# Kernel optimization log

Hardware: AMD Instinct MI355X
Metric: run time of the kernel (lower is better)

Reference implementation:

```python
import jax, jax.numpy as jnp
import numpy as np

BETA = 0.9       # membrane decay factor
THRESHOLD = 1.0  # firing threshold
ALPHA = 2.0      # atan surrogate slope (snntorch default)

@jax.custom_vjp
def spike(x):
    # Heaviside spike on (mem - threshold)
    return (x > 0).astype(x.dtype)

def _spike_fwd(x):
    return (x > 0).astype(x.dtype), x

def _spike_bwd(x, g):
    # atan surrogate: d spk / d x = (alpha/2) / (1 + (pi/2 * alpha * x)^2)
    return (g * (ALPHA / 2.0) / (1.0 + (jnp.pi / 2.0 * ALPHA * x) ** 2),)

spike.defvjp(_spike_fwd, _spike_bwd)


def snn_forward(x, params):
    """x: (T, B, F_in); params: list of (W[out,in], b[out]).
    Returns (spike_record (T,B,out), final membrane (B,out)).
    Dropout is identity (eval mode). LIF: mem=beta*mem+cur; spk=H(mem-thr); mem-=spk*thr."""
    B = x.shape[1]
    mems0 = tuple(jnp.zeros((B, W.shape[0]), x.dtype) for W, _ in params)

    def step(mems, xt):
        h = xt
        new_mems = []
        for (W, b), m in zip(params, mems):
            cur = h @ W.T + b                 # (B, out)
            m = BETA * m + cur                # leaky integrate
            s = spike(m - THRESHOLD)          # fire
            m = m - s * THRESHOLD             # subtract reset
            new_mems.append(m)
            h = s                             # spikes feed next layer
        return tuple(new_mems), (h, new_mems[-1])

    _, (spks, mem_rec) = jax.lax.scan(step, mems0, x)
    return spks, mem_rec[-1]


def _linear_init(key, out_f, in_f):
    k1, k2 = jax.random.split(key)
    bound = 1.0 / np.sqrt(in_f)
    W = jax.random.uniform(k1, (out_f, in_f), jnp.float32, -bound, bound)
    b = jax.random.uniform(k2, (out_f,), jnp.float32, -bound, bound)
    return W, b


def setup_inputs() -> dict:
    key = jax.random.key(0)
    ks = jax.random.split(key, 4)
    T, B = 25, 256
    sizes = [1024, 2048, 2048, 1024]
    x = jax.random.normal(ks[0], (T, B, sizes[0]), jnp.float32)
    w0, b0 = _linear_init(ks[1], sizes[1], sizes[0])
    w1, b1 = _linear_init(ks[2], sizes[2], sizes[1])
    w2, b2 = _linear_init(ks[3], sizes[3], sizes[2])
    return {"x": x, "w0": w0, "b0": b0, "w1": w1, "b1": b1, "w2": w2, "b2": b2}


def reference(x, w0, b0, w1, b1, w2, b2):
    return snn_forward(x, [(w0, b0), (w1, b1), (w2, b2)])
```

## Files before the change

### kernel.cpp

```cpp
#include <hip/hip_runtime.h>
#include <hip/hip_bf16.h>

typedef __bf16 bf16;
typedef __bf16 bf16x4 __attribute__((ext_vector_type(4)));
typedef __bf16 bf16x8 __attribute__((ext_vector_type(8)));
typedef float  f32x4  __attribute__((ext_vector_type(4)));

#define DEVFN static __device__ __forceinline__

static constexpr int T_STEPS = 25;
static constexpr int BATCH   = 256;
static constexpr int MROWS   = T_STEPS * BATCH;

DEVFN void llds16(const void* g, void* l) {
    __builtin_amdgcn_global_load_lds(
        (const __attribute__((address_space(1))) void*)g,
        (__attribute__((address_space(3))) void*)l, 16, 0, 0);
}

DEVFN void split3_chunk(const float* src, bf16* p0, bf16* p1, bf16* p2, int i) {
    float4 v = *(const float4*)(src + i);
    float vv[4] = {v.x, v.y, v.z, v.w};
    bf16x4 a, b, c;
#pragma unroll
    for (int k = 0; k < 4; ++k) {
        bf16 h0 = (bf16)vv[k];
        float r1 = vv[k] - (float)h0;
        bf16 h1 = (bf16)r1;
        float r2 = r1 - (float)h1;
        a[k] = h0; b[k] = h1; c[k] = (bf16)r2;
    }
    *(bf16x4*)(p0 + i) = a;
    *(bf16x4*)(p1 + i) = b;
    *(bf16x4*)(p2 + i) = c;
}

DEVFN void split2_chunk(const float* src, bf16* p0, bf16* p1, int i) {
    float4 v = *(const float4*)(src + i);
    float vv[4] = {v.x, v.y, v.z, v.w};
    bf16x4 a, b;
#pragma unroll
    for (int k = 0; k < 4; ++k) {
        bf16 h0 = (bf16)vv[k];
        a[k] = h0; b[k] = (bf16)(vv[k] - (float)h0);
    }
    *(bf16x4*)(p0 + i) = a;
    *(bf16x4*)(p1 + i) = b;
}

static constexpr int SB_W0 = 2048;
static constexpr int SB_W1 = 4096;
static constexpr int SB_W2 = 2048;
static constexpr int SB_X  = 6400;

__global__ void split_all(const float* __restrict__ w0, bf16* w0p0, bf16* w0p1, bf16* w0p2,
                          const float* __restrict__ w1, bf16* w1p0, bf16* w1p1, bf16* w1p2,
                          const float* __restrict__ w2, bf16* w2p0, bf16* w2p1,
                          const float* __restrict__ x,  bf16* xp0,  bf16* xp1,  bf16* xp2) {
    int b = blockIdx.x;
    if (b < SB_W0) {
        split3_chunk(w0, w0p0, w0p1, w0p2, b * 1024 + threadIdx.x * 4);
    } else if (b < SB_W0 + SB_W1) {
        split3_chunk(w1, w1p0, w1p1, w1p2, (b - SB_W0) * 1024 + threadIdx.x * 4);
    } else if (b < SB_W0 + SB_W1 + SB_W2) {
        split2_chunk(w2, w2p0, w2p1, (b - SB_W0 - SB_W1) * 1024 + threadIdx.x * 4);
    } else {
        split3_chunk(x, xp0, xp1, xp2, (b - SB_W0 - SB_W1 - SB_W2) * 1024 + threadIdx.x * 4);
    }
}


struct TileCtx { int t, lane, wm, wn, bm, bn, fr, fkS, fk64a, fk64b, cr, cc; };

DEVFN TileCtx make_ctx512() {
    TileCtx x;
    x.t = threadIdx.x; x.lane = x.t & 63;
    int wv = x.t >> 6;
    x.wm = (wv >> 1) * 64;
    x.wn = (wv & 1) * 64;
    x.bm = blockIdx.x * 256; x.bn = blockIdx.y * 128;
    x.fr  = x.lane & 15;
    int g = x.lane >> 4;
    x.fkS   = (g ^ ((x.lane >> 1) & 3)) * 16;
    x.fk64a = ((0 * 4 + g) ^ (x.lane & 7)) * 16;
    x.fk64b = ((1 * 4 + g) ^ (x.lane & 7)) * 16;
    x.cr = (x.lane >> 4) * 4; x.cc = x.lane & 15;
    return x;
}

template <int ROWS, int BK>
DEVFN void stageP(const bf16* g, bf16* s, int base_row, int K, int k0, int t) {
    constexpr int CPR  = BK / 8;
    constexpr int ITER = ROWS * CPR / 512;
#pragma unroll
    for (int r = 0; r < ITER; ++r) {
        int c    = t + r * 512;
        int row  = c / CPR;
        int slot = c % CPR;
        int src  = (BK == 32) ? (slot ^ ((row >> 1) & 3))
                              : (slot ^ (row & 7));
        llds16(g + (size_t)(base_row + row) * K + k0 + src * 8,
               (bf16*)((char*)s + (c >> 6) * 1024));
    }
}

template <int BK>
DEVFN void frag4(bf16x8* f, const bf16* s, int wrow, int fr, int fkS) {
#pragma unroll
    for (int i = 0; i < 4; ++i)
        f[i] = *(const bf16x8*)((const char*)s + (wrow + i * 16 + fr) * (2 * BK) + fkS);
}

DEVFN void mfma16(f32x4 (&acc)[4][4], const bf16x8* a, const bf16x8* b) {
#pragma unroll
    for (int i = 0; i < 4; ++i)
#pragma unroll
        for (int j = 0; j < 4; ++j)
            acc[i][j] = __builtin_amdgcn_mfma_f32_16x16x32_bf16(a[i], b[j], acc[i][j], 0, 0, 0);
}

DEVFN void epilogue(const f32x4 (&accM)[4][4], const f32x4 (&accS)[4][4],
                    const float* bias, float* C, int N, const TileCtx& x) {
#pragma unroll
    for (int j = 0; j < 4; ++j) {
        int col   = x.bn + x.wn + j * 16 + x.cc;
        double bv = (double)bias[col];
#pragma unroll
        for (int i = 0; i < 4; ++i) {
            int row0 = x.bm + x.wm + i * 16 + x.cr;
#pragma unroll
            for (int r = 0; r < 4; ++r) {
                double v = (double)accM[i][j][r] + (double)accS[i][j][r] + bv;
                C[(size_t)(row0 + r) * N + col] = (float)v;
            }
        }
    }
}

template <int MODE>
__global__ __launch_bounds__(512, 2)
void gemm_ph(const bf16* __restrict__ A0, const bf16* __restrict__ A1,
             const bf16* __restrict__ A2, const bf16* __restrict__ B0,
             const bf16* __restrict__ B1, const bf16* __restrict__ B2,
             const float* __restrict__ bias, float* __restrict__ C,
             int M, int N, int K) {
    constexpr int BK  = (MODE == 0) ? 32 : 64;
    constexpr int NA  = (MODE == 0) ? 3 : 1;
    constexpr int NB  = (MODE == 2) ? 2 : 3;
    constexpr int APL = 256 * BK;
    constexpr int BPL = 128 * BK;
    constexpr int BUF = NA * APL + NB * BPL;
    __shared__ __align__(1024) bf16 lds[2 * BUF];

    TileCtx x = make_ctx512();
    f32x4 accM[4][4] = {}, accS[4][4] = {};

    auto pA = [&](int p, int i) { return lds + p * BUF + i * APL; };
    auto pB = [&](int p, int i) { return lds + p * BUF + NA * APL + i * BPL; };

    auto stage_all = [&](int p, int k0) {
        stageP<256, BK>(A0, pA(p, 0), x.bm, K, k0, x.t);
        if constexpr (MODE == 0) {
            stageP<256, BK>(A1, pA(p, 1), x.bm, K, k0, x.t);
            stageP<256, BK>(A2, pA(p, 2), x.bm, K, k0, x.t);
        }
        stageP<128, BK>(B0, pB(p, 0), x.bn, K, k0, x.t);
        stageP<128, BK>(B1, pB(p, 1), x.bn, K, k0, x.t);
        if constexpr (NB == 3) stageP<128, BK>(B2, pB(p, 2), x.bn, K, k0, x.t);
    };

    stage_all(0, 0);
    __syncthreads();

    const int NT = K / BK;
    int p = 0;
    for (int tt = 0; tt < NT; ++tt, p ^= 1) {
        if (tt + 1 < NT) stage_all(p ^ 1, (tt + 1) * BK);

        bf16x8 a[4], b0f[4], b1f[4], b2f[4];
        if constexpr (MODE == 0) {
            frag4<32>(a,   pA(p, 0), x.wm, x.fr, x.fkS);
            frag4<32>(b0f, pB(p, 0), x.wn, x.fr, x.fkS);
            mfma16(accM, a, b0f);
            frag4<32>(b1f, pB(p, 1), x.wn, x.fr, x.fkS);
            mfma16(accS, a, b1f);
            frag4<32>(b2f, pB(p, 2), x.wn, x.fr, x.fkS);
            mfma16(accS, a, b2f);
            frag4<32>(a, pA(p, 1), x.wm, x.fr, x.fkS);
            mfma16(accS, a, b0f);
            mfma16(accS, a, b1f);
            frag4<32>(a, pA(p, 2), x.wm, x.fr, x.fkS);
            mfma16(accS, a, b0f);
        } else {
#pragma unroll
            for (int kh = 0; kh < 2; ++kh) {
                const int fk = kh ? x.fk64b : x.fk64a;
                frag4<64>(a,   pA(p, 0), x.wm, x.fr, fk);
                frag4<64>(b0f, pB(p, 0), x.wn, x.fr, fk);
                mfma16(accM, a, b0f);
                frag4<64>(b1f, pB(p, 1), x.wn, x.fr, fk);
                mfma16(accS, a, b1f);
                if constexpr (NB == 3) {
                    frag4<64>(b2f, pB(p, 2), x.wn, x.fr, fk);
                    mfma16(accS, a, b2f);
                }
            }
        }
        __syncthreads();
    }
    epilogue(accM, accS, bias, C, N, x);
}

template <int F>
__global__ void lif_hidden(const float* __restrict__ cur, bf16* __restrict__ spk) {
    const int tid = blockIdx.x * 256 + threadIdx.x;
    double m = 0.0;
    size_t off = tid;
#pragma unroll
    for (int t = 0; t < T_STEPS; ++t) {
        m = 0.9 * m + (double)cur[off];
        bool s = (m - 1.0) > 0.0;
        spk[off] = (bf16)(s ? 1.0f : 0.0f);
        if (s) m -= 1.0;
        off += (size_t)BATCH * F;
    }
}

__global__ void lif_out(const float* __restrict__ cur, float* __restrict__ out) {
    const int tid = blockIdx.x * 256 + threadIdx.x;
    double m = 0.0;
    size_t off = tid;
#pragma unroll
    for (int t = 0; t < T_STEPS; ++t) {
        m = 0.9 * m + (double)cur[off];
        bool s = (m - 1.0) > 0.0;
        out[off] = s ? 1.0f : 0.0f;
        if (s) m -= 1.0;
        off += (size_t)BATCH * 1024;
    }
    out[(size_t)T_STEPS * BATCH * 1024 + tid] = (float)m;
}

extern "C" void kernel_launch(void* const* d_in, const int* in_sizes, int n_in,
                              void* d_out, int out_size, void* d_ws, size_t ws_size,
                              hipStream_t stream) {
    const float* xin = (const float*)d_in[0];
    const float* w0  = (const float*)d_in[1];
    const float* b0  = (const float*)d_in[2];
    const float* w1  = (const float*)d_in[3];
    const float* b1  = (const float*)d_in[4];
    const float* w2  = (const float*)d_in[5];
    const float* b2  = (const float*)d_in[6];
    float* out = (float*)d_out;

    constexpr size_t NW0 = 2048 * 1024;
    constexpr size_t NW1 = 2048 * 2048;
    constexpr size_t NW2 = 1024 * 2048;
    constexpr size_t NX  = (size_t)MROWS * 1024;
    constexpr size_t NH  = (size_t)MROWS * 2048;

    char* ws = (char*)d_ws;
    size_t off = 0;
    auto carve = [&](size_t bytes) { char* p = ws + off; off += bytes; return p; };

    bf16* w1p0 = (bf16*)carve(NW1 * 2);
    bf16* w1p1 = (bf16*)carve(NW1 * 2);
    bf16* w1p2 = (bf16*)carve(NW1 * 2);
    bf16* w2p0 = (bf16*)carve(NW2 * 2);
    bf16* w2p1 = (bf16*)carve(NW2 * 2);
    char* pool = carve(2 * NH * 2);
    bf16* w0p0 = (bf16*)pool;
    bf16* w0p1 = w0p0 + NW0;
    bf16* w0p2 = w0p1 + NW0;
    bf16* xp0  = w0p2 + NW0;
    bf16* xp1  = xp0 + NX;
    bf16* xp2  = xp1 + NX;
    bf16* s0   = (bf16*)pool;
    bf16* s1   = s0 + NH;
    float* cur = (float*)carve(NH * 4);
    if (ws_size < off) return;

    split_all<<<SB_W0 + SB_W1 + SB_W2 + SB_X, 256, 0, stream>>>(
        w0, w0p0, w0p1, w0p2, w1, w1p0, w1p1, w1p2,
        w2, w2p0, w2p1, xin, xp0, xp1, xp2);

    gemm_ph<0><<<dim3(25, 16), 512, 0, stream>>>(xp0, xp1, xp2, w0p0, w0p1, w0p2,
                                                 b0, cur, MROWS, 2048, 1024);
    lif_hidden<2048><<<(BATCH * 2048) / 256, 256, 0, stream>>>(cur, s0);

    gemm_ph<1><<<dim3(25, 16), 512, 0, stream>>>(s0, nullptr, nullptr, w1p0, w1p1, w1p2,
                                                 b1, cur, MROWS, 2048, 2048);
    lif_hidden<2048><<<(BATCH * 2048) / 256, 256, 0, stream>>>(cur, s1);

    gemm_ph<2><<<dim3(25, 8), 512, 0, stream>>>(s1, nullptr, nullptr, w2p0, w2p1, nullptr,
                                                b2, cur, MROWS, 1024, 2048);
    lif_out<<<(BATCH * 1024) / 256, 256, 0, stream>>>(cur, out);
}
```

Baseline: 470.2 us.

## Interleave next-tile LDS prefetch with MFMA and precompute staging offsets

The global-to-LDS loads for the next K tile are no longer issued as one block at the top of each iteration. They are now spread between fragment reads and MFMA groups so memory issue overlaps with matrix math. Per-thread global offsets for the staging loads are computed once before the loop instead of being recomputed every tile. This costs a few extra registers for the offset arrays and makes the instruction schedule more dependent on the compiler.

```diff
diff --git a/kernel.cpp b/kernel.cpp
--- a/kernel.cpp
+++ b/kernel.cpp
@@ -88,22 +88,6 @@
     return x;
 }
 
-template <int ROWS, int BK>
-DEVFN void stageP(const bf16* g, bf16* s, int base_row, int K, int k0, int t) {
-    constexpr int CPR  = BK / 8;
-    constexpr int ITER = ROWS * CPR / 512;
-#pragma unroll
-    for (int r = 0; r < ITER; ++r) {
-        int c    = t + r * 512;
-        int row  = c / CPR;
-        int slot = c % CPR;
-        int src  = (BK == 32) ? (slot ^ ((row >> 1) & 3))
-                              : (slot ^ (row & 7));
-        llds16(g + (size_t)(base_row + row) * K + k0 + src * 8,
-               (bf16*)((char*)s + (c >> 6) * 1024));
-    }
-}
-
 template <int BK>
 DEVFN void frag4(bf16x8* f, const bf16* s, int wrow, int fr, int fkS) {
 #pragma unroll
@@ -145,6 +129,9 @@
              const float* __restrict__ bias, float* __restrict__ C,
              int M, int N, int K) {
     constexpr int BK  = (MODE == 0) ? 32 : 64;
+    constexpr int CPR = BK / 8;
+    constexpr int AIT = CPR / 2;
+    constexpr int BIT = CPR / 4;
     constexpr int NA  = (MODE == 0) ? 3 : 1;
     constexpr int NB  = (MODE == 2) ? 2 : 3;
     constexpr int APL = 256 * BK;
@@ -158,32 +145,54 @@
     auto pA = [&](int p, int i) { return lds + p * BUF + i * APL; };
     auto pB = [&](int p, int i) { return lds + p * BUF + NA * APL + i * BPL; };
 
-    auto stage_all = [&](int p, int k0) {
-        stageP<256, BK>(A0, pA(p, 0), x.bm, K, k0, x.t);
-        if constexpr (MODE == 0) {
-            stageP<256, BK>(A1, pA(p, 1), x.bm, K, k0, x.t);
-            stageP<256, BK>(A2, pA(p, 2), x.bm, K, k0, x.t);
-        }
-        stageP<128, BK>(B0, pB(p, 0), x.bn, K, k0, x.t);
-        stageP<128, BK>(B1, pB(p, 1), x.bn, K, k0, x.t);
-        if constexpr (NB == 3) stageP<128, BK>(B2, pB(p, 2), x.bn, K, k0, x.t);
+    size_t offA[AIT], offB[BIT];
+#pragma unroll
+    for (int r = 0; r < AIT; ++r) {
+        int c = x.t + r * 512, row = c / CPR, slot = c % CPR;
+        int src = (BK == 32) ? (slot ^ ((row >> 1) & 3)) : (slot ^ (row & 7));
+        offA[r] = (size_t)(x.bm + row) * K + src * 8;
+    }
+#pragma unroll
+    for (int r = 0; r < BIT; ++r) {
+        int c = x.t + r * 512, row = c / CPR, slot = c % CPR;
+        int src = (BK == 32) ? (slot ^ ((row >> 1) & 3)) : (slot ^ (row & 7));
+        offB[r] = (size_t)(x.bn + row) * K + src * 8;
+    }
+    auto stA = [&](const bf16* g, bf16* s, int k0) {
+#pragma unroll
+        for (int r = 0; r < AIT; ++r)
+            llds16(g + offA[r] + k0, (char*)s + ((x.t + r * 512) >> 6) * 1024);
     };
-
-    stage_all(0, 0);
+    auto stB = [&](const bf16* g, bf16* s, int k0) {
+#pragma unroll
+        for (int r = 0; r < BIT; ++r)
+            llds16(g + offB[r] + k0, (char*)s + ((x.t + r * 512) >> 6) * 1024);
+    };
+
+    stA(A0, pA(0, 0), 0);
+    if constexpr (MODE == 0) { stA(A1, pA(0, 1), 0); stA(A2, pA(0, 2), 0); }
+    stB(B0, pB(0, 0), 0);
+    stB(B1, pB(0, 1), 0);
+    if constexpr (NB == 3) stB(B2, pB(0, 2), 0);
     __syncthreads();
 
     const int NT = K / BK;
     int p = 0;
     for (int tt = 0; tt < NT; ++tt, p ^= 1) {
-        if (tt + 1 < NT) stage_all(p ^ 1, (tt + 1) * BK);
-
+        const int  q  = p ^ 1;
+        const int  kn = (tt + 1) * BK;
+        const bool pf = (tt + 1 < NT);
         bf16x8 a[4], b0f[4], b1f[4], b2f[4];
+
         if constexpr (MODE == 0) {
             frag4<32>(a,   pA(p, 0), x.wm, x.fr, x.fkS);
             frag4<32>(b0f, pB(p, 0), x.wn, x.fr, x.fkS);
-            mfma16(accM, a, b0f);
+            if (pf) stA(A0, pA(q, 0), kn);
+            mfma16(accM, a, b0f);
+            if (pf) { stA(A1, pA(q, 1), kn); stA(A2, pA(q, 2), kn); }
             frag4<32>(b1f, pB(p, 1), x.wn, x.fr, x.fkS);
             mfma16(accS, a, b1f);
+            if (pf) { stB(B0, pB(q, 0), kn); stB(B1, pB(q, 1), kn); stB(B2, pB(q, 2), kn); }
             frag4<32>(b2f, pB(p, 2), x.wn, x.fr, x.fkS);
             mfma16(accS, a, b2f);
             frag4<32>(a, pA(p, 1), x.wm, x.fr, x.fkS);
@@ -191,20 +200,37 @@
             mfma16(accS, a, b1f);
             frag4<32>(a, pA(p, 2), x.wm, x.fr, x.fkS);
             mfma16(accS, a, b0f);
+        } else if constexpr (MODE == 1) {
+            frag4<64>(a,   pA(p, 0), x.wm, x.fr, x.fk64a);
+            frag4<64>(b0f, pB(p, 0), x.wn, x.fr, x.fk64a);
+            if (pf) stA(A0, pA(q, 0), kn);
+            mfma16(accM, a, b0f);
+            if (pf) { stB(B0, pB(q, 0), kn); stB(B1, pB(q, 1), kn); }
+            frag4<64>(b1f, pB(p, 1), x.wn, x.fr, x.fk64a);
+            mfma16(accS, a, b1f);
+            if (pf) stB(B2, pB(q, 2), kn);
+            frag4<64>(b2f, pB(p, 2), x.wn, x.fr, x.fk64a);
+            mfma16(accS, a, b2f);
+            frag4<64>(a,   pA(p, 0), x.wm, x.fr, x.fk64b);
+            frag4<64>(b0f, pB(p, 0), x.wn, x.fr, x.fk64b);
+            mfma16(accM, a, b0f);
+            frag4<64>(b1f, pB(p, 1), x.wn, x.fr, x.fk64b);
+            mfma16(accS, a, b1f);
+            frag4<64>(b2f, pB(p, 2), x.wn, x.fr, x.fk64b);
+            mfma16(accS, a, b2f);
         } else {
-#pragma unroll
-            for (int kh = 0; kh < 2; ++kh) {
-                const int fk = kh ? x.fk64b : x.fk64a;
-                frag4<64>(a,   pA(p, 0), x.wm, x.fr, fk);
-                frag4<64>(b0f, pB(p, 0), x.wn, x.fr, fk);
-                mfma16(accM, a, b0f);
-                frag4<64>(b1f, pB(p, 1), x.wn, x.fr, fk);
-                mfma16(accS, a, b1f);
-                if constexpr (NB == 3) {
-                    frag4<64>(b2f, pB(p, 2), x.wn, x.fr, fk);
-                    mfma16(accS, a, b2f);
-                }
-            }
+            frag4<64>(a,   pA(p, 0), x.wm, x.fr, x.fk64a);
+            frag4<64>(b0f, pB(p, 0), x.wn, x.fr, x.fk64a);
+            if (pf) stA(A0, pA(q, 0), kn);
+            mfma16(accM, a, b0f);
+            if (pf) { stB(B0, pB(q, 0), kn); stB(B1, pB(q, 1), kn); }
+            frag4<64>(b1f, pB(p, 1), x.wn, x.fr, x.fk64a);
+            mfma16(accS, a, b1f);
+            frag4<64>(a,   pA(p, 0), x.wm, x.fr, x.fk64b);
+            frag4<64>(b0f, pB(p, 0), x.wn, x.fr, x.fk64b);
+            mfma16(accM, a, b0f);
+            frag4<64>(b1f, pB(p, 1), x.wn, x.fr, x.fk64b);
+            mfma16(accS, a, b1f);
         }
         __syncthreads();
     }
```

Measured after the change: 465.2 us. Within noise of the previous version (-1.1%).
